# Kernel optimization log

Hardware: AMD Instinct MI355X
Metric: run time of the kernel (lower is better)

## Reference

```python
import jax, jax.numpy as jnp
import numpy as np

TOP_K = 2
ROUTED_SCALING = 1.0


def setup_inputs() -> dict:
    key = jax.random.key(0)
    k1, k2, k3, k4 = jax.random.split(key, 4)
    S, B, H = 1024, 2, 1024
    E, FFN = 8, 1408
    return {
        "hidden_states": jax.random.normal(k1, (S, B, H), dtype=jnp.float32),
        "gate_w": jax.random.normal(k2, (E, H), dtype=jnp.float32) * 0.02,
        "w1": jax.random.normal(k3, (E, H, 2 * FFN), dtype=jnp.float32) * 0.02,
        "w2": jax.random.normal(k4, (E, FFN, H), dtype=jnp.float32) * 0.02,
    }


def reference(hidden_states, gate_w, w1, w2):
    # hidden_states: [S, B, H] -> transpose(0,1) as in MoELayer.forward
    x = jnp.transpose(hidden_states, (1, 0, 2))  # [B, S, H]
    B, S, H = x.shape
    E = gate_w.shape[0]
    xt = x.reshape(-1, H)  # [T, H], T = B*S
    T = xt.shape[0]

    # --- TopKGate ('greedy', softmax scoring) ---
    scores = jax.nn.softmax(xt @ gate_w.T, axis=-1)  # [T, E]
    topk_w, topk_idx = jax.lax.top_k(scores, TOP_K)  # [T, K]
    # norm_topk_prob: normalize the top-k weights
    topk_w = topk_w / (jnp.sum(topk_w, axis=-1, keepdims=True) + 1e-20)
    topk_w = topk_w * ROUTED_SCALING

    # Sparse combine weights [T, E] (zero for non-selected experts)
    combine = jnp.zeros((T, E), dtype=xt.dtype)
    combine = combine.at[jnp.arange(T)[:, None], topk_idx].set(topk_w)

    # --- Experts: per-expert swiglu MLP, weighted combine ---
    # Equivalent math to dispatch -> per-expert grouped GEMM -> combine:
    # non-selected experts contribute with weight 0.
    out = jnp.zeros_like(xt)
    for e in range(E):
        h = xt @ w1[e]                      # [T, 2*FFN]
        g, u = jnp.split(h, 2, axis=-1)
        y = (jax.nn.silu(g) * u) @ w2[e]    # [T, H]
        out = out + combine[:, e:e + 1] * y

    out = out.reshape(B, S, H)
    return jnp.transpose(out, (1, 0, 2))  # back to [S, B, H]
```

## Files before the change

kernel.cpp:

```cpp
#include <hip/hip_runtime.h>
#include <hip/hip_bf16.h>

#define S_      1024
#define B_      2
#define H_      1024
#define E_      8
#define FFN_    1408
#define TWO_FFN 2816
#define T_      2048
#define MAXSLOTS 5120
#define NB_T1   (44 * 16 * 8)
#define NB_T2   (16 * 22 * 8)
#define NB_CONV 512
#define NB_PREP (NB_T1 + NB_T2 + NB_CONV)

typedef float  f32x4 __attribute__((ext_vector_type(4)));
typedef short  s16x8 __attribute__((ext_vector_type(8)));

__device__ __forceinline__ unsigned short f2bf(float f) {
    unsigned u = __float_as_uint(f);
    u += 0x7fffu + ((u >> 16) & 1u);
    return (unsigned short)(u >> 16);
}
__device__ __forceinline__ void async16(const void* g, void* l) {
    __builtin_amdgcn_global_load_lds(
        (const __attribute__((address_space(1))) unsigned int*)(unsigned long long)g,
        (__attribute__((address_space(3))) unsigned int*)(unsigned long long)l,
        16, 0, 0);
}
__device__ __forceinline__ size_t xrow_off(int t) {
    return (size_t)(t & (S_ - 1)) * (B_ * H_) + (size_t)(t >> 10) * H_;
}

__device__ __forceinline__ void transpose_body(const float* __restrict__ ip,
                                               unsigned short* __restrict__ op,
                                               int R, int C, int r0, int c0,
                                               float (*lds)[65], int tid) {
    int q = tid & 15, rr = tid >> 4;
#pragma unroll
    for (int i = 0; i < 4; i++) {
        int r = rr + 16 * i;
        const float4 v = *(const float4*)(ip + (size_t)(r0 + r) * C + c0 + q * 4);
        lds[q * 4 + 0][r] = v.x;
        lds[q * 4 + 1][r] = v.y;
        lds[q * 4 + 2][r] = v.z;
        lds[q * 4 + 3][r] = v.w;
    }
    __syncthreads();
    int oq = tid & 7, cc = tid >> 3;
#pragma unroll
    for (int i = 0; i < 2; i++) {
        int c = cc + 32 * i;
        const float* row = &lds[c][oq * 8];
        unsigned short o[8];
#pragma unroll
        for (int j = 0; j < 8; j++) o[j] = f2bf(row[j]);
        *(uint4*)(op + (size_t)(c0 + c) * R + r0 + oq * 8) = *(const uint4*)o;
    }
}

__global__ void k_prep(const float* __restrict__ hs, const float* __restrict__ gw,
                       const float* __restrict__ w1, const float* __restrict__ w2,
                       unsigned short* __restrict__ xb,
                       unsigned short* __restrict__ w1bt, unsigned short* __restrict__ w2bt,
                       int* __restrict__ topkI, float* __restrict__ topkW) {
    __shared__ float tile[64][65];
    int bx = blockIdx.x, tid = threadIdx.x;
    if (bx < NB_T1) {
        int e = bx / (44 * 16), rem = bx % (44 * 16);
        int c0 = (rem % 44) * 64, r0 = (rem / 44) * 64;
        transpose_body(w1 + (size_t)e * (H_ * TWO_FFN), w1bt + (size_t)e * (H_ * TWO_FFN),
                       H_, TWO_FFN, r0, c0, tile, tid);
        return;
    }
    if (bx < NB_T1 + NB_T2) {
        int b2 = bx - NB_T1;
        int e = b2 / (16 * 22), rem = b2 % (16 * 22);
        int c0 = (rem % 16) * 64, r0 = (rem / 16) * 64;
        transpose_body(w2 + (size_t)e * (FFN_ * H_), w2bt + (size_t)e * (FFN_ * H_),
                       FFN_, H_, r0, c0, tile, tid);
        return;
    }
    int cb = bx - (NB_T1 + NB_T2);
    int wid = tid >> 6, lane = tid & 63;
    int t = cb * 4 + wid;
    const float* xr = hs + xrow_off(t);
    unsigned short* xo = xb + (size_t)t * H_;
    float acc[E_];
#pragma unroll
    for (int e = 0; e < E_; e++) acc[e] = 0.f;
#pragma unroll
    for (int p = 0; p < 4; p++) {
        int h = p * 256 + lane * 4;
        const float4 v = *(const float4*)(xr + h);
        unsigned short o[4] = { f2bf(v.x), f2bf(v.y), f2bf(v.z), f2bf(v.w) };
        *(uint2*)(xo + h) = *(const uint2*)o;
#pragma unroll
        for (int e = 0; e < E_; e++) {
            const float4 g = *(const float4*)(gw + e * H_ + h);
            acc[e] += v.x * g.x + v.y * g.y + v.z * g.z + v.w * g.w;
        }
    }
#pragma unroll
    for (int e = 0; e < E_; e++)
        for (int off = 32; off > 0; off >>= 1) acc[e] += __shfl_down(acc[e], off);
    if (lane == 0) {
        float l0 = -1e30f, l1 = -1e30f; int i0 = 0, i1 = 0;
#pragma unroll
        for (int e = 0; e < E_; e++) {
            float v = acc[e];
            if (v > l0)      { l1 = l0; i1 = i0; l0 = v; i0 = e; }
            else if (v > l1) { l1 = v;  i1 = e; }
        }
        float p1 = expf(l1 - l0);
        float w0 = 1.f / (1.f + p1);
        float w1s = 1.f - w0;
        topkI[2 * t] = i0; topkI[2 * t + 1] = i1;
        topkW[2 * t] = w0; topkW[2 * t + 1] = w1s;
    }
}

__global__ void k_routeassign(const int* __restrict__ topkI, const float* __restrict__ topkW,
                              int* __restrict__ ctrl, int* __restrict__ perm,
                              int* __restrict__ slotOfTok) {
    __shared__ int s_wcnt[4][E_];
    __shared__ int s_base[E_];
    __shared__ int s_cur[E_];
    int tid = threadIdx.x, wid = tid >> 6, lane = tid & 63;
    int cnt[E_];
#pragma unroll
    for (int j = 0; j < E_; j++) cnt[j] = 0;
    for (int i = tid; i < 2 * T_; i += 256) {
        int e = topkI[i];
#pragma unroll
        for (int j = 0; j < E_; j++) cnt[j] += (e == j);
    }
#pragma unroll
    for (int j = 0; j < E_; j++)
        for (int off = 32; off > 0; off >>= 1) cnt[j] += __shfl_down(cnt[j], off);
    if (lane == 0) {
#pragma unroll
        for (int j = 0; j < E_; j++) s_wcnt[wid][j] = cnt[j];
    }
    __syncthreads();
    if (tid == 0) {
        int b = 0;
        for (int e = 0; e < E_; e++) {
            int n = s_wcnt[0][e] + s_wcnt[1][e] + s_wcnt[2][e] + s_wcnt[3][e];
            int ntile = (n + 127) >> 7;
            s_base[e] = b;
            ctrl[40 + e] = ntile;
            ctrl[48 + e] = b;
            b += ntile * 128;
        }
#pragma unroll
        for (int e = 0; e < E_; e++) s_cur[e] = 0;
    }
    __syncthreads();
    for (int s = tid; s < MAXSLOTS; s += 256) perm[s] = 0;
    __syncthreads();
    for (int t = tid; t < T_; t += 256) {
#pragma unroll
        for (int k = 0; k < 2; k++) {
            int e = topkI[2 * t + k];
            int pos = atomicAdd(&s_cur[e], 1);
            int slot = s_base[e] + pos;
            perm[slot] = t;
            slotOfTok[2 * t + k] = slot;
        }
    }
}

__global__ __launch_bounds__(256) void k_gemm1(
    const unsigned short* __restrict__ xb, const unsigned short* __restrict__ w1bt,
    const int* __restrict__ ctrl, const int* __restrict__ perm,
    unsigned short* __restrict__ A2) {
    int e  = blockIdx.x & 7;
    int ct = blockIdx.x >> 3;
    int ti = blockIdx.y;
    if (ti >= ctrl[40 + e]) return;
    int slot0 = ctrl[48 + e] + ti * 128;
    __shared__ __align__(16) unsigned short smem[2 * 128 * 64];
    unsigned short* As = smem;
    unsigned short* Bs = smem + 128 * 64;
    int tid = threadIdx.x, wid = tid >> 6, lane = tid & 63;

    const unsigned short* aPtr[4];
    const unsigned short* bPtr[4];
    unsigned short* lA[4];
    unsigned short* lB[4];
#pragma unroll
    for (int i = 0; i < 4; i++) {
        int c = (wid * 4 + i) * 64 + lane;
        int r = c >> 3;
        int qd = (c & 7) ^ (r & 7);
        int col8 = qd * 8;
        int tok = perm[slot0 + r];
        int gr = (r < 64) ? (ct * 64 + r) : (FFN_ + ct * 64 + (r - 64));
        aPtr[i] = xb + (size_t)tok * H_ + col8;
        bPtr[i] = w1bt + ((size_t)e * TWO_FFN + gr) * H_ + col8;
        lA[i] = As + (size_t)c * 8;
        lB[i] = Bs + (size_t)c * 8;
    }
    f32x4 acc[4][4];
#pragma unroll
    for (int mi = 0; mi < 4; mi++)
#pragma unroll
        for (int ni = 0; ni < 4; ni++) acc[mi][ni] = (f32x4){0.f, 0.f, 0.f, 0.f};
    int wm = wid & 1, wn = wid >> 1;
    int rowB = wm * 64, colB = wn * 64;
    int sw = (lane & 7) << 3;

    for (int k0 = 0; k0 < H_; k0 += 64) {
#pragma unroll
        for (int i = 0; i < 4; i++) { async16(aPtr[i] + k0, lA[i]); async16(bPtr[i] + k0, lB[i]); }
        __syncthreads();
#pragma unroll
        for (int kk = 0; kk < 64; kk += 32) {
            int kr = (kk + ((lane >> 4) << 3)) ^ sw;
            s16x8 af[4], bf[4];
#pragma unroll
            for (int mi = 0; mi < 4; mi++) af[mi] = *(const s16x8*)&As[(rowB + mi * 16 + (lane & 15)) * 64 + kr];
#pragma unroll
            for (int ni = 0; ni < 4; ni++) bf[ni] = *(const s16x8*)&Bs[(colB + ni * 16 + (lane & 15)) * 64 + kr];
#pragma unroll
            for (int mi = 0; mi < 4; mi++)
#pragma unroll
                for (int ni = 0; ni < 4; ni++)
                    acc[mi][ni] = __builtin_amdgcn_mfma_f32_16x16x32_bf16(af[mi], bf[ni], acc[mi][ni], 0, 0, 0);
        }
        __syncthreads();
    }
    float* upLds = (float*)smem;
    if (wn == 1) {
#pragma unroll
        for (int mi = 0; mi < 4; mi++)
#pragma unroll
            for (int ni = 0; ni < 4; ni++)
#pragma unroll
                for (int r = 0; r < 4; r++) {
                    int m = rowB + mi * 16 + (lane >> 4) * 4 + r;
                    int u = ni * 16 + (lane & 15);
                    upLds[m * 64 + u] = acc[mi][ni][r];
                }
    }
    __syncthreads();
    if (wn == 0) {
#pragma unroll
        for (int mi = 0; mi < 4; mi++)
#pragma unroll
            for (int r = 0; r < 4; r++) {
                int m = rowB + mi * 16 + (lane >> 4) * 4 + r;
                unsigned short* arow = A2 + (size_t)(slot0 + m) * FFN_ + ct * 64;
#pragma unroll
                for (int ni = 0; ni < 4; ni++) {
                    int gl = ni * 16 + (lane & 15);
                    float g = acc[mi][ni][r];
                    float u = upLds[m * 64 + gl];
                    float s = g / (1.f + expf(-g));
                    arow[gl] = f2bf(s * u);
                }
            }
    }
}

__global__ __launch_bounds__(256) void k_gemm2(
    const unsigned short* __restrict__ A2, const unsigned short* __restrict__ w2bt,
    const int* __restrict__ ctrl, unsigned short* __restrict__ Yp) {
    int e  = blockIdx.x & 7;
    int ct = blockIdx.x >> 3;
    int ti = blockIdx.y;
    if (ti >= ctrl[40 + e]) return;
    int slot0 = ctrl[48 + e] + ti * 128;
    int ks    = blockIdx.z;
    __shared__ __align__(16) unsigned short As[128 * 64];
    __shared__ __align__(16) unsigned short Bs[128 * 64];
    int tid = threadIdx.x, wid = tid >> 6, lane = tid & 63;

    const unsigned short* aPtr[4];
    const unsigned short* bPtr[4];
    unsigned short* lA[4];
    unsigned short* lB[4];
#pragma unroll
    for (int i = 0; i < 4; i++) {
        int c = (wid * 4 + i) * 64 + lane;
        int r = c >> 3;
        int qd = (c & 7) ^ (r & 7);
        int col8 = qd * 8;
        aPtr[i] = A2 + (size_t)(slot0 + r) * FFN_ + col8;
        bPtr[i] = w2bt + ((size_t)e * H_ + ct * 128 + r) * FFN_ + col8;
        lA[i] = As + (size_t)c * 8;
        lB[i] = Bs + (size_t)c * 8;
    }
    f32x4 acc[4][4];
#pragma unroll
    for (int mi = 0; mi < 4; mi++)
#pragma unroll
        for (int ni = 0; ni < 4; ni++) acc[mi][ni] = (f32x4){0.f, 0.f, 0.f, 0.f};
    int wm = wid & 1, wn = wid >> 1;
    int rowB = wm * 64, colB = wn * 64;
    int sw = (lane & 7) << 3;

    int kbeg = ks * (FFN_ / 2), kend = kbeg + FFN_ / 2;
    for (int k0 = kbeg; k0 < kend; k0 += 64) {
#pragma unroll
        for (int i = 0; i < 4; i++) { async16(aPtr[i] + k0, lA[i]); async16(bPtr[i] + k0, lB[i]); }
        __syncthreads();
#pragma unroll
        for (int kk = 0; kk < 64; kk += 32) {
            int kr = (kk + ((lane >> 4) << 3)) ^ sw;
            s16x8 af[4], bf[4];
#pragma unroll
            for (int mi = 0; mi < 4; mi++) af[mi] = *(const s16x8*)&As[(rowB + mi * 16 + (lane & 15)) * 64 + kr];
#pragma unroll
            for (int ni = 0; ni < 4; ni++) bf[ni] = *(const s16x8*)&Bs[(colB + ni * 16 + (lane & 15)) * 64 + kr];
#pragma unroll
            for (int mi = 0; mi < 4; mi++)
#pragma unroll
                for (int ni = 0; ni < 4; ni++)
                    acc[mi][ni] = __builtin_amdgcn_mfma_f32_16x16x32_bf16(af[mi], bf[ni], acc[mi][ni], 0, 0, 0);
        }
        __syncthreads();
    }
    unsigned short* yp = Yp + (size_t)ks * MAXSLOTS * H_;
#pragma unroll
    for (int mi = 0; mi < 4; mi++)
#pragma unroll
        for (int r = 0; r < 4; r++) {
            int m = rowB + mi * 16 + (lane >> 4) * 4 + r;
#pragma unroll
            for (int ni = 0; ni < 4; ni++) {
                int n = colB + ni * 16 + (lane & 15);
                yp[(size_t)(slot0 + m) * H_ + ct * 128 + n] = f2bf(acc[mi][ni][r]);
            }
        }
}

__global__ void k_combine(const unsigned short* __restrict__ Yp, const int* __restrict__ slotOfTok,
                          const float* __restrict__ topkW, float* __restrict__ out) {
    int t = blockIdx.x;
    int h = threadIdx.x * 4;
    int sA = slotOfTok[2 * t], sB = slotOfTok[2 * t + 1];
    float wA = topkW[2 * t],   wB = topkW[2 * t + 1];
    const unsigned short* pA0 = Yp + (size_t)sA * H_ + h;
    const unsigned short* pA1 = Yp + ((size_t)MAXSLOTS + sA) * H_ + h;
    const unsigned short* pB0 = Yp + (size_t)sB * H_ + h;
    const unsigned short* pB1 = Yp + ((size_t)MAXSLOTS + sB) * H_ + h;
    unsigned short a0[4], a1[4], b0[4], b1[4];
    *(uint2*)a0 = *(const uint2*)pA0;
    *(uint2*)a1 = *(const uint2*)pA1;
    *(uint2*)b0 = *(const uint2*)pB0;
    *(uint2*)b1 = *(const uint2*)pB1;
    float4 r;
    float* rp = (float*)&r;
#pragma unroll
    for (int i = 0; i < 4; i++) {
        float av = __uint_as_float(((unsigned)a0[i]) << 16) + __uint_as_float(((unsigned)a1[i]) << 16);
        float bv = __uint_as_float(((unsigned)b0[i]) << 16) + __uint_as_float(((unsigned)b1[i]) << 16);
        rp[i] = wA * av + wB * bv;
    }
    *(float4*)(out + xrow_off(t) + h) = r;
}

extern "C" void kernel_launch(void* const* d_in, const int* in_sizes, int n_in,
                              void* d_out, int out_size, void* d_ws, size_t ws_size,
                              hipStream_t stream) {
    (void)in_sizes; (void)n_in; (void)ws_size; (void)out_size;
    const float* hs = (const float*)d_in[0];
    const float* gw = (const float*)d_in[1];
    const float* w1 = (const float*)d_in[2];
    const float* w2 = (const float*)d_in[3];
    float* out = (float*)d_out;
    char* ws = (char*)d_ws;

    int*            ctrl   = (int*)ws;
    int*            topkI  = (int*)(ws + (16u << 10));
    float*          topkW  = (float*)(ws + (48u << 10));
    int*            perm   = (int*)(ws + (80u << 10));
    int*            slotOfTok = (int*)(ws + (144u << 10));
    unsigned short* xb    = (unsigned short*)(ws + (1ull  << 20));
    unsigned short* w1bt  = (unsigned short*)(ws + (5ull  << 20));
    unsigned short* Yp    = (unsigned short*)(ws + (5ull << 20));
    unsigned short* w2bt  = (unsigned short*)(ws + (49ull << 20));
    unsigned short* A2    = (unsigned short*)(ws + (71ull << 20));

    k_prep<<<NB_PREP, 256, 0, stream>>>(hs, gw, w1, w2, xb, w1bt, w2bt, topkI, topkW);
    k_routeassign<<<1, 256, 0, stream>>>(topkI, topkW, ctrl, perm, slotOfTok);
    k_gemm1<<<dim3(8 * (FFN_ / 64), 16), 256, 0, stream>>>(xb, w1bt, ctrl, perm, A2);
    k_gemm2<<<dim3(8 * (H_ / 128), 16, 2), 256, 0, stream>>>(A2, w2bt, ctrl, Yp);
    k_combine<<<2048, 256, 0, stream>>>(Yp, slotOfTok, topkW, out);
}
```

Baseline: 273.9 us.

## Fuse weight fp32-to-bf16 transpose into GEMM B-tile staging

Drops the separate pass that transposed and converted w1/w2 to bf16 in global memory. Each GEMM block now reads fp32 weight rows directly, converts them to bf16 in registers, and writes them transposed into swizzled LDS. Block indices are also reordered so that blocks sharing an expert and column tile are grouped together, which may improve L2 reuse. The cost is that every token tile re-reads fp32 weights (twice the bytes of bf16) and does synchronous loads instead of async global-to-LDS copies, while the large bf16 weight write/read round trip is removed.

```diff
diff --git a/kernel.cpp b/kernel.cpp
--- a/kernel.cpp
+++ b/kernel.cpp
@@ -9,10 +9,7 @@
 #define TWO_FFN 2816
 #define T_      2048
 #define MAXSLOTS 5120
-#define NB_T1   (44 * 16 * 8)
-#define NB_T2   (16 * 22 * 8)
 #define NB_CONV 512
-#define NB_PREP (NB_T1 + NB_T2 + NB_CONV)
 
 typedef float  f32x4 __attribute__((ext_vector_type(4)));
 typedef short  s16x8 __attribute__((ext_vector_type(8)));
@@ -32,56 +29,36 @@
     return (size_t)(t & (S_ - 1)) * (B_ * H_) + (size_t)(t >> 10) * H_;
 }
 
-__device__ __forceinline__ void transpose_body(const float* __restrict__ ip,
-                                               unsigned short* __restrict__ op,
-                                               int R, int C, int r0, int c0,
-                                               float (*lds)[65], int tid) {
-    int q = tid & 15, rr = tid >> 4;
-#pragma unroll
-    for (int i = 0; i < 4; i++) {
-        int r = rr + 16 * i;
-        const float4 v = *(const float4*)(ip + (size_t)(r0 + r) * C + c0 + q * 4);
-        lds[q * 4 + 0][r] = v.x;
-        lds[q * 4 + 1][r] = v.y;
-        lds[q * 4 + 2][r] = v.z;
-        lds[q * 4 + 3][r] = v.w;
-    }
-    __syncthreads();
-    int oq = tid & 7, cc = tid >> 3;
-#pragma unroll
-    for (int i = 0; i < 2; i++) {
-        int c = cc + 32 * i;
-        const float* row = &lds[c][oq * 8];
-        unsigned short o[8];
-#pragma unroll
-        for (int j = 0; j < 8; j++) o[j] = f2bf(row[j]);
-        *(uint4*)(op + (size_t)(c0 + c) * R + r0 + oq * 8) = *(const uint4*)o;
+__device__ __forceinline__ void stage_b_f32(const float* __restrict__ p, size_t Cs,
+                                            unsigned* const bw[4]) {
+    float4 v[8];
+#pragma unroll
+    for (int r = 0; r < 8; r++) v[r] = *(const float4*)(p + (size_t)r * Cs);
+#pragma unroll
+    for (int jh = 0; jh < 2; jh++) {
+        const float4 a0 = v[4 * jh + 0], a1 = v[4 * jh + 1];
+        const float4 b0 = v[4 * jh + 2], b1 = v[4 * jh + 3];
+        unsigned ua[4], ub[4];
+        ua[0] = f2bf(a0.x) | ((unsigned)f2bf(a1.x) << 16);
+        ua[1] = f2bf(a0.y) | ((unsigned)f2bf(a1.y) << 16);
+        ua[2] = f2bf(a0.z) | ((unsigned)f2bf(a1.z) << 16);
+        ua[3] = f2bf(a0.w) | ((unsigned)f2bf(a1.w) << 16);
+        ub[0] = f2bf(b0.x) | ((unsigned)f2bf(b1.x) << 16);
+        ub[1] = f2bf(b0.y) | ((unsigned)f2bf(b1.y) << 16);
+        ub[2] = f2bf(b0.z) | ((unsigned)f2bf(b1.z) << 16);
+        ub[3] = f2bf(b0.w) | ((unsigned)f2bf(b1.w) << 16);
+#pragma unroll
+        for (int i = 0; i < 4; i++) {
+            uint2 w; w.x = ua[i]; w.y = ub[i];
+            *(uint2*)(bw[i] + 2 * jh) = w;
+        }
     }
 }
 
 __global__ void k_prep(const float* __restrict__ hs, const float* __restrict__ gw,
-                       const float* __restrict__ w1, const float* __restrict__ w2,
                        unsigned short* __restrict__ xb,
-                       unsigned short* __restrict__ w1bt, unsigned short* __restrict__ w2bt,
                        int* __restrict__ topkI, float* __restrict__ topkW) {
-    __shared__ float tile[64][65];
-    int bx = blockIdx.x, tid = threadIdx.x;
-    if (bx < NB_T1) {
-        int e = bx / (44 * 16), rem = bx % (44 * 16);
-        int c0 = (rem % 44) * 64, r0 = (rem / 44) * 64;
-        transpose_body(w1 + (size_t)e * (H_ * TWO_FFN), w1bt + (size_t)e * (H_ * TWO_FFN),
-                       H_, TWO_FFN, r0, c0, tile, tid);
-        return;
-    }
-    if (bx < NB_T1 + NB_T2) {
-        int b2 = bx - NB_T1;
-        int e = b2 / (16 * 22), rem = b2 % (16 * 22);
-        int c0 = (rem % 16) * 64, r0 = (rem / 16) * 64;
-        transpose_body(w2 + (size_t)e * (FFN_ * H_), w2bt + (size_t)e * (FFN_ * H_),
-                       FFN_, H_, r0, c0, tile, tid);
-        return;
-    }
-    int cb = bx - (NB_T1 + NB_T2);
+    int cb = blockIdx.x, tid = threadIdx.x;
     int wid = tid >> 6, lane = tid & 63;
     int t = cb * 4 + wid;
     const float* xr = hs + xrow_off(t);
@@ -172,12 +149,14 @@
 }
 
 __global__ __launch_bounds__(256) void k_gemm1(
-    const unsigned short* __restrict__ xb, const unsigned short* __restrict__ w1bt,
+    const unsigned short* __restrict__ xb, const float* __restrict__ w1,
     const int* __restrict__ ctrl, const int* __restrict__ perm,
     unsigned short* __restrict__ A2) {
-    int e  = blockIdx.x & 7;
-    int ct = blockIdx.x >> 3;
-    int ti = blockIdx.y;
+    int b  = blockIdx.x;
+    int p  = ((b >> 7) << 3) | (b & 7);
+    int ti = (b >> 3) & 15;
+    int e  = p / 22;
+    int ct = p - e * 22;
     if (ti >= ctrl[40 + e]) return;
     int slot0 = ctrl[48 + e] + ti * 128;
     __shared__ __align__(16) unsigned short smem[2 * 128 * 64];
@@ -186,22 +165,26 @@
     int tid = threadIdx.x, wid = tid >> 6, lane = tid & 63;
 
     const unsigned short* aPtr[4];
-    const unsigned short* bPtr[4];
     unsigned short* lA[4];
-    unsigned short* lB[4];
 #pragma unroll
     for (int i = 0; i < 4; i++) {
         int c = (wid * 4 + i) * 64 + lane;
         int r = c >> 3;
         int qd = (c & 7) ^ (r & 7);
-        int col8 = qd * 8;
         int tok = perm[slot0 + r];
-        int gr = (r < 64) ? (ct * 64 + r) : (FFN_ + ct * 64 + (r - 64));
-        aPtr[i] = xb + (size_t)tok * H_ + col8;
-        bPtr[i] = w1bt + ((size_t)e * TWO_FFN + gr) * H_ + col8;
+        aPtr[i] = xb + (size_t)tok * H_ + qd * 8;
         lA[i] = As + (size_t)c * 8;
-        lB[i] = Bs + (size_t)c * 8;
-    }
+    }
+    int h1 = tid >> 7, kp = (tid >> 4) & 7, nq = tid & 15;
+    int rb = h1 * 64 + nq * 4;
+    const float* bsrc = w1 + (size_t)e * (H_ * TWO_FFN)
+                        + (h1 ? (FFN_ + ct * 64) : (ct * 64)) + nq * 4
+                        + (size_t)(kp * 8) * TWO_FFN;
+    unsigned* bw[4];
+#pragma unroll
+    for (int i = 0; i < 4; i++)
+        bw[i] = (unsigned*)Bs + (rb + i) * 32 + ((kp ^ ((rb & 7) + i)) << 2);
+
     f32x4 acc[4][4];
 #pragma unroll
     for (int mi = 0; mi < 4; mi++)
@@ -213,7 +196,8 @@
 
     for (int k0 = 0; k0 < H_; k0 += 64) {
 #pragma unroll
-        for (int i = 0; i < 4; i++) { async16(aPtr[i] + k0, lA[i]); async16(bPtr[i] + k0, lB[i]); }
+        for (int i = 0; i < 4; i++) async16(aPtr[i] + k0, lA[i]);
+        stage_b_f32(bsrc + (size_t)k0 * TWO_FFN, TWO_FFN, bw);
         __syncthreads();
 #pragma unroll
         for (int kk = 0; kk < 64; kk += 32) {
@@ -265,33 +249,40 @@
 }
 
 __global__ __launch_bounds__(256) void k_gemm2(
-    const unsigned short* __restrict__ A2, const unsigned short* __restrict__ w2bt,
+    const unsigned short* __restrict__ A2, const float* __restrict__ w2,
     const int* __restrict__ ctrl, unsigned short* __restrict__ Yp) {
-    int e  = blockIdx.x & 7;
-    int ct = blockIdx.x >> 3;
-    int ti = blockIdx.y;
+    int b  = blockIdx.x;
+    int p  = ((b >> 7) << 3) | (b & 7);
+    int ti = (b >> 3) & 15;
+    int e  = p >> 4;
+    int ct = (p >> 1) & 7;
+    int ks = p & 1;
     if (ti >= ctrl[40 + e]) return;
     int slot0 = ctrl[48 + e] + ti * 128;
-    int ks    = blockIdx.z;
     __shared__ __align__(16) unsigned short As[128 * 64];
     __shared__ __align__(16) unsigned short Bs[128 * 64];
     int tid = threadIdx.x, wid = tid >> 6, lane = tid & 63;
 
     const unsigned short* aPtr[4];
-    const unsigned short* bPtr[4];
     unsigned short* lA[4];
-    unsigned short* lB[4];
 #pragma unroll
     for (int i = 0; i < 4; i++) {
         int c = (wid * 4 + i) * 64 + lane;
         int r = c >> 3;
         int qd = (c & 7) ^ (r & 7);
-        int col8 = qd * 8;
-        aPtr[i] = A2 + (size_t)(slot0 + r) * FFN_ + col8;
-        bPtr[i] = w2bt + ((size_t)e * H_ + ct * 128 + r) * FFN_ + col8;
+        aPtr[i] = A2 + (size_t)(slot0 + r) * FFN_ + qd * 8;
         lA[i] = As + (size_t)c * 8;
-        lB[i] = Bs + (size_t)c * 8;
-    }
+    }
+    int h1 = tid >> 7, kp = (tid >> 4) & 7, nq = tid & 15;
+    int rb = h1 * 64 + nq * 4;
+    const float* bsrc = w2 + (size_t)e * (FFN_ * H_)
+                        + ct * 128 + h1 * 64 + nq * 4
+                        + (size_t)(kp * 8) * H_;
+    unsigned* bw[4];
+#pragma unroll
+    for (int i = 0; i < 4; i++)
+        bw[i] = (unsigned*)Bs + (rb + i) * 32 + ((kp ^ ((rb & 7) + i)) << 2);
+
     f32x4 acc[4][4];
 #pragma unroll
     for (int mi = 0; mi < 4; mi++)
@@ -304,7 +295,8 @@
     int kbeg = ks * (FFN_ / 2), kend = kbeg + FFN_ / 2;
     for (int k0 = kbeg; k0 < kend; k0 += 64) {
 #pragma unroll
-        for (int i = 0; i < 4; i++) { async16(aPtr[i] + k0, lA[i]); async16(bPtr[i] + k0, lB[i]); }
+        for (int i = 0; i < 4; i++) async16(aPtr[i] + k0, lA[i]);
+        stage_b_f32(bsrc + (size_t)k0 * H_, H_, bw);
         __syncthreads();
 #pragma unroll
         for (int kk = 0; kk < 64; kk += 32) {
@@ -379,14 +371,12 @@
     int*            perm   = (int*)(ws + (80u << 10));
     int*            slotOfTok = (int*)(ws + (144u << 10));
     unsigned short* xb    = (unsigned short*)(ws + (1ull  << 20));
-    unsigned short* w1bt  = (unsigned short*)(ws + (5ull  << 20));
-    unsigned short* Yp    = (unsigned short*)(ws + (5ull << 20));
-    unsigned short* w2bt  = (unsigned short*)(ws + (49ull << 20));
-    unsigned short* A2    = (unsigned short*)(ws + (71ull << 20));
-
-    k_prep<<<NB_PREP, 256, 0, stream>>>(hs, gw, w1, w2, xb, w1bt, w2bt, topkI, topkW);
+    unsigned short* A2    = (unsigned short*)(ws + (8ull  << 20));
+    unsigned short* Yp    = (unsigned short*)(ws + (24ull << 20));
+
+    k_prep<<<NB_CONV, 256, 0, stream>>>(hs, gw, xb, topkI, topkW);
     k_routeassign<<<1, 256, 0, stream>>>(topkI, topkW, ctrl, perm, slotOfTok);
-    k_gemm1<<<dim3(8 * (FFN_ / 64), 16), 256, 0, stream>>>(xb, w1bt, ctrl, perm, A2);
-    k_gemm2<<<dim3(8 * (H_ / 128), 16, 2), 256, 0, stream>>>(A2, w2bt, ctrl, Yp);
+    k_gemm1<<<dim3(22 * 128), 256, 0, stream>>>(xb, w1, ctrl, perm, A2);
+    k_gemm2<<<dim3(16 * 128), 256, 0, stream>>>(A2, w2, ctrl, Yp);
     k_combine<<<2048, 256, 0, stream>>>(Yp, slotOfTok, topkW, out);
 }
```

Result: slower. 303.3 us (+10.7%).
